# Kernel optimization log

Hardware: AMD Instinct MI355X
Metric: run time of the kernel (lower is better)

The kernel has to match this reference:

```python
import jax, jax.numpy as jnp
import numpy as np
from jax import lax

THRESHOLD = 0.95
NUM_HEADS = 32
Q_HEAD_DIM = 96
K_DIM = 1024
EPS = 1e-8


def dynamic_token_replacement(emb, thr=THRESHOLD):
    """Greedy sequential merge: token j is replaced by the first earlier
    *unused* token i with cosine sim > thr. emb: (S, D) -> (S, D)."""
    S = emb.shape[0]
    norm = jnp.maximum(jnp.linalg.norm(emb, axis=-1, keepdims=True), EPS)
    n = emb / norm
    sim = n @ n.T  # (S, S) cosine similarity
    idx = jnp.arange(S)

    def step(carry, xs):
        used, rep = carry
        i, row = xs
        # i can only absorb later, unused tokens, and only if i itself is unused
        cand = (idx > i) & (row > thr) & (~used) & (~used[i])
        rep = jnp.where(cand, i, rep)
        used = used | cand
        return (used, rep), None

    (used, rep), _ = lax.scan(step, (jnp.zeros(S, bool), idx), (idx, sim))
    return emb[rep]


def setup_inputs() -> dict:
    key = jax.random.key(0)
    ks = jax.random.split(key, 7)
    B, S, D = 2, 1024, 3072
    s = 0.02
    return {
        "hidden_states": jax.random.normal(ks[0], (B, S, D), jnp.float32),
        "Wq": jax.random.normal(ks[1], (D, D), jnp.float32) * s,
        "bq": jnp.zeros((D,), jnp.float32),
        "Wk": jax.random.normal(ks[2], (D, K_DIM), jnp.float32) * s,
        "bk": jnp.zeros((K_DIM,), jnp.float32),
        "Wv": jax.random.normal(ks[3], (D, K_DIM), jnp.float32) * s,
        "bv": jnp.zeros((K_DIM,), jnp.float32),
        "Wqk": jax.random.normal(ks[4], (Q_HEAD_DIM, K_DIM), jnp.float32) * s,
        "bqk": jnp.zeros((K_DIM,), jnp.float32),
        "Wo": jax.random.normal(ks[5], (K_DIM, D), jnp.float32) * s,
        "bo": jnp.zeros((D,), jnp.float32),
    }


def reference(hidden_states, Wq, bq, Wk, bk, Wv, bv, Wqk, bqk, Wo, bo):
    B, S, D = hidden_states.shape
    q = hidden_states @ Wq + bq                      # (B, S, 3072)
    k = hidden_states @ Wk + bk                      # (B, S, 1024)
    v = hidden_states @ Wv + bv                      # (B, S, 1024)

    q = q.reshape(B, S, NUM_HEADS, Q_HEAD_DIM).transpose(0, 2, 1, 3)  # (B, H, S, 96)
    q_new = q @ Wqk + bqk                            # (B, H, S, 1024)

    new_k = jax.vmap(dynamic_token_replacement)(k)   # (B, S, 1024)
    new_v = jax.vmap(dynamic_token_replacement)(v)   # (B, S, 1024)

    scale = 1.0 / jnp.sqrt(jnp.float32(K_DIM))
    scores = jnp.einsum('bhsk,btk->bhst', q_new, new_k) * scale  # (B, H, S, S)
    attn = jax.nn.softmax(scores, axis=-1)
    out = jnp.einsum('bhst,btk->bhsk', attn, new_v)  # (B, H, S, 1024)
    out = out.mean(axis=1)                           # (B, S, 1024)
    return out @ Wo + bo                             # (B, S, 3072)
```

## Files before the change

### kernel.cpp

```cpp
#include <hip/hip_runtime.h>
#include <hip/hip_bf16.h>
#include <stdint.h>

#define BATCH 2
#define SEQ   1024
#define DIM   3072
#define KDIM  1024
#define NHEAD 32
#define HDQ   96
#define THR_SIM 0.95f

typedef unsigned short u16;
typedef __attribute__((ext_vector_type(8))) short short8;
typedef __attribute__((ext_vector_type(4))) float f32x4;

typedef const __attribute__((address_space(1))) unsigned int* gas_ptr;
typedef __attribute__((address_space(3))) unsigned int* las_ptr;

__device__ __forceinline__ void glds16(const u16* g, u16* l) {
  __builtin_amdgcn_global_load_lds((gas_ptr)g, (las_ptr)l, 16, 0, 0);
}

__device__ __forceinline__ u16 f2bf(float f) {
  union { float f; unsigned u; } v; v.f = f;
  unsigned r = v.u + 0x7FFFu + ((v.u >> 16) & 1u);
  return (u16)(r >> 16);
}
__device__ __forceinline__ float bf2f(u16 x) {
  union { unsigned u; float f; } v; v.u = ((unsigned)x) << 16; return v.f;
}

__device__ __forceinline__ f32x4 mfma16(short8 a, short8 b, f32x4 c) {
  return __builtin_amdgcn_mfma_f32_16x16x32_bf16(a, b, c, 0, 0, 0);
}

__global__ void k_cvt_bf16(const float* __restrict__ in, u16* __restrict__ out, int n4) {
  int i = blockIdx.x * blockDim.x + threadIdx.x;
  if (i < n4) {
    float4 v = ((const float4*)in)[i];
    ushort4 o;
    o.x = f2bf(v.x); o.y = f2bf(v.y); o.z = f2bf(v.z); o.w = f2bf(v.w);
    ((ushort4*)out)[i] = o;
  }
}

__global__ void k_tr_f32_bf16(const float* __restrict__ in, u16* __restrict__ out, int R, int C) {
  __shared__ float t[32][33];
  int c0 = blockIdx.x * 32, r0 = blockIdx.y * 32;
  int tx = threadIdx.x, ty = threadIdx.y;
  #pragma unroll
  for (int k = 0; k < 4; ++k)
    t[ty + 8 * k][tx] = in[(size_t)(r0 + ty + 8 * k) * C + c0 + tx];
  __syncthreads();
  #pragma unroll
  for (int k = 0; k < 4; ++k)
    out[(size_t)(c0 + ty + 8 * k) * R + r0 + tx] = f2bf(t[tx][ty + 8 * k]);
}

__global__ void k_tr_bf16(const u16* __restrict__ in, u16* __restrict__ out,
                          int ldin, int ldout, long long zsIn, long long zsOut) {
  __shared__ u16 t[32][33];
  const u16* ib = in + (size_t)blockIdx.z * zsIn;
  u16* ob = out + (size_t)blockIdx.z * zsOut;
  int c0 = blockIdx.x * 32, r0 = blockIdx.y * 32;
  int tx = threadIdx.x, ty = threadIdx.y;
  #pragma unroll
  for (int k = 0; k < 4; ++k)
    t[ty + 8 * k][tx] = ib[(size_t)(r0 + ty + 8 * k) * ldin + c0 + tx];
  __syncthreads();
  #pragma unroll
  for (int k = 0; k < 4; ++k)
    ob[(size_t)(c0 + ty + 8 * k) * ldout + r0 + tx] = t[tx][ty + 8 * k];
}

__global__ void k_build_wqke(const float* __restrict__ Wqk, const float* __restrict__ bqk,
                             u16* __restrict__ out) {
  const int n = blockIdx.x;
  const int c = threadIdx.x * 4;
  float4 v;
  if (n < 96)       v = *(const float4*)(Wqk + (size_t)n * KDIM + c);
  else if (n == 96) v = *(const float4*)(bqk + c);
  else              v = make_float4(0.f, 0.f, 0.f, 0.f);
  ushort4 o;
  o.x = f2bf(v.x); o.y = f2bf(v.y); o.z = f2bf(v.z); o.w = f2bf(v.w);
  *(ushort4*)(out + (size_t)n * KDIM + c) = o;
}

__global__ void k_bkv(const float* __restrict__ bk, const float* __restrict__ bv,
                      float* __restrict__ out) {
  int i = blockIdx.x * 256 + threadIdx.x;
  if (i < 2048) out[i] = (i < 1024) ? bk[i] : bv[i - 1024];
}

template<bool OUT_BF16, bool BIAS>
__global__ __launch_bounds__(256, 3) void k_gemm_bt(
    const u16* __restrict__ A, const u16* __restrict__ Bt, void* __restrict__ Cv,
    const float* __restrict__ bias, int M, int N, int K,
    int lda, int ldb, int ldc,
    long long bsAH, long long bsAL, long long bsBH, long long bsBL,
    long long bsCH, long long bsCL)
{
  const int zb = blockIdx.y, zH = zb >> 1, zL = zb & 1;
  A  += (size_t)(zH * bsAH + zL * bsAL);
  Bt += (size_t)(zH * bsBH + zL * bsBL);
  u16*   Cb16 = (u16*)Cv + (size_t)(zH * bsCH + zL * bsCL);
  float* Cf32 = (float*)Cv + (size_t)(zH * bsCH + zL * bsCL);

  __shared__ u16 Ls[2][24 * 512];
  const int nt = N >> 6;
  int bid = blockIdx.x;
  {
    const int nwg = gridDim.x;
    const int qq = nwg >> 3, rr = nwg & 7;
    const int x = bid & 7, pos = bid >> 3;
    bid = (x < rr ? x * (qq + 1) : rr * (qq + 1) + (x - rr) * qq) + pos;
  }
  const int tm = bid / nt, tn = bid % nt;
  const int tid = threadIdx.x, lane = tid & 63, wid = tid >> 6;
  const int wr = wid >> 1, wc = wid & 1, li = lane & 15, lg = lane >> 4;

  const int rsub = lane >> 3;
  const int cbe = ((lane & 7) ^ rsub) << 3;
  const u16* gp[6];
  int lof[6];
  #pragma unroll
  for (int j = 0; j < 6; ++j) {
    const int ci = wid * 6 + j;
    lof[j] = ci << 9;
    if (ci < 16) gp[j] = A + (size_t)(tm * 128 + ci * 8 + rsub) * lda + cbe;
    else         gp[j] = Bt + (size_t)(tn * 64 + (ci - 16) * 8 + rsub) * ldb + cbe;
  }

  f32x4 acc[4][2];
  #pragma unroll
  for (int a = 0; a < 4; ++a)
    #pragma unroll
    for (int b = 0; b < 2; ++b) acc[a][b] = (f32x4){0.f, 0.f, 0.f, 0.f};

  const int nk = K >> 6;
  #pragma unroll
  for (int j = 0; j < 6; ++j) { glds16(gp[j], Ls[0] + lof[j]); gp[j] += 64; }
  __syncthreads();

  for (int kt = 0; kt < nk; ++kt) {
    const u16* Lc = Ls[kt & 1];
    if (kt + 1 < nk) {
      u16* Ln = Ls[(kt + 1) & 1];
      #pragma unroll
      for (int j = 0; j < 6; ++j) { glds16(gp[j], Ln + lof[j]); gp[j] += 64; }
    }
    short8 af[2][4], bfv[2][2];
    #pragma unroll
    for (int ks = 0; ks < 2; ++ks) {
      const int sw = (((ks * 4 + lg) ^ (li & 7)) << 3);
      #pragma unroll
      for (int mf = 0; mf < 4; ++mf)
        af[ks][mf] = *(const short8*)(Lc + (wr * 64 + mf * 16 + li) * 64 + sw);
      #pragma unroll
      for (int nf = 0; nf < 2; ++nf)
        bfv[ks][nf] = *(const short8*)(Lc + 8192 + (wc * 32 + nf * 16 + li) * 64 + sw);
    }
    #pragma unroll
    for (int ks = 0; ks < 2; ++ks)
      #pragma unroll
      for (int mf = 0; mf < 4; ++mf)
        #pragma unroll
        for (int nf = 0; nf < 2; ++nf)
          acc[mf][nf] = mfma16(af[ks][mf], bfv[ks][nf], acc[mf][nf]);
    __syncthreads();
  }
  #pragma unroll
  for (int mf = 0; mf < 4; ++mf) {
    #pragma unroll
    for (int nf = 0; nf < 2; ++nf) {
      const int col = tn * 64 + wc * 32 + nf * 16 + li;
      const float bb = BIAS ? bias[col] : 0.f;
      #pragma unroll
      for (int j = 0; j < 4; ++j) {
        const int row = tm * 128 + wr * 64 + mf * 16 + lg * 4 + j;
        const float v = acc[mf][nf][j] + bb;
        if (OUT_BF16) Cb16[(size_t)row * ldc + col] = f2bf(v);
        else          Cf32[(size_t)row * ldc + col] = v;
      }
    }
  }
}

__global__ void k_norms(const float* __restrict__ gram, float* __restrict__ nrm,
                        int* __restrict__ anyCnt) {
  const int s = blockIdx.x, j = threadIdx.x;
  const float* g = gram + (size_t)s * SEQ * SEQ;
  float nj = fmaxf(sqrtf(fmaxf(g[(size_t)j * SEQ + j], 0.f)), 1e-8f);
  nrm[s * SEQ + j] = nj;
  if (j == 0) anyCnt[s] = 0;
}

__global__ void k_rowany(const float* __restrict__ gram, const float* __restrict__ nrm,
                         unsigned char* __restrict__ rowAny, int* __restrict__ anyCnt) {
  const int i = blockIdx.x, s = blockIdx.y, t = threadIdx.x;
  const float* g = gram + (size_t)s * SEQ * SEQ + (size_t)i * SEQ;
  const float* nr = nrm + s * SEQ;
  const float ni = nr[i];
  int any = 0;
  for (int j = i + 1 + t; j < SEQ; j += 256)
    any |= (g[j] > THR_SIM * ni * nr[j]) ? 1 : 0;
  any = __any(any) ? 1 : 0;
  __shared__ int sh[4];
  if ((t & 63) == 0) sh[t >> 6] = any;
  __syncthreads();
  if (t == 0) {
    int a = sh[0] | sh[1] | sh[2] | sh[3];
    rowAny[s * SEQ + i] = (unsigned char)a;
    if (a) atomicAdd(&anyCnt[s], 1);
  }
}

__global__ __launch_bounds__(1024) void k_scan_replace(
    const float* __restrict__ gram, const float* __restrict__ nrmG,
    const unsigned char* __restrict__ rowAnyG, const int* __restrict__ anyCnt,
    u16* __restrict__ kvbase)
{
  const int s = blockIdx.x;
  if (anyCnt[s] == 0) return;
  const float* g = gram + (size_t)s * SEQ * SEQ;
  u16* dat = kvbase + (size_t)(s >> 1) * (2048 * 2048 / 2) * 2 + (size_t)(s & 1) * 1024;
  const int ldr = 2048;
  __shared__ float nrm[SEQ];
  __shared__ unsigned char used[SEQ];
  __shared__ unsigned char rowAny[SEQ];
  __shared__ short rep[SEQ];
  const int j = threadIdx.x;
  nrm[j] = nrmG[s * SEQ + j];
  rowAny[j] = rowAnyG[s * SEQ + j];
  used[j] = 0; rep[j] = (short)j;
  __syncthreads();
  for (int i = 0; i < SEQ - 1; ++i) {
    if (rowAny[i] && !used[i]) {
      const float t = THR_SIM * nrm[i];
      if (j > i && !used[j] && g[(size_t)i * SEQ + j] > t * nrm[j]) {
        used[j] = 1; rep[j] = (short)i;
      }
      __syncthreads();
    }
  }
  __syncthreads();
  const int src = rep[j];
  if (src != j) {
    for (int c = 0; c < KDIM; c += 8)
      *(uint4*)(dat + (size_t)j * ldr + c) = *(const uint4*)(dat + (size_t)src * ldr + c);
  }
}

__global__ __launch_bounds__(1024, 4) void k_attn3(
    const u16* __restrict__ q_bf, const u16* __restrict__ KKTe,
    u16* __restrict__ pbarP)
{
  const int bid = blockIdx.x;
  const int xcd = bid & 7, qt = bid >> 3;
  const int b = xcd >> 2, pg = xcd & 3;
  const int q0 = qt * 16;
  const int tid = threadIdx.x, lane = tid & 63, w = tid >> 6;
  const int li = lane & 15, lg = lane >> 4;

  __shared__ float bkkl[1024];
  __shared__ float2 red[2][16][16];

  const u16* KKb = KKTe + (size_t)b * SEQ * 128;
  bkkl[tid] = bf2f(KKb[(size_t)tid * 128 + 96]);

  short8 ak[4][3];
  #pragma unroll
  for (int kf = 0; kf < 4; ++kf)
    #pragma unroll
    for (int ks = 0; ks < 3; ++ks)
      ak[kf][ks] = *(const short8*)(KKb + (size_t)(w * 64 + kf * 16 + li) * 128 + ks * 32 + lg * 8);

  f32x4 accm[4];
  #pragma unroll
  for (int kf = 0; kf < 4; ++kf) accm[kf] = (f32x4){0.f, 0.f, 0.f, 0.f};
  __syncthreads();

  const u16* qrow = q_bf + (size_t)(b * SEQ + q0 + li) * DIM + pg * 8 * HDQ;

  for (int hh = 0; hh < 8; ++hh) {
    const u16* qp = qrow + hh * HDQ;
    f32x4 acc[4];
    #pragma unroll
    for (int kf = 0; kf < 4; ++kf) acc[kf] = (f32x4){0.f, 0.f, 0.f, 0.f};
    #pragma unroll
    for (int ks = 0; ks < 3; ++ks) {
      short8 bq = *(const short8*)(qp + ks * 32 + lg * 8);
      #pragma unroll
      for (int kf = 0; kf < 4; ++kf)
        acc[kf] = mfma16(ak[kf][ks], bq, acc[kf]);
    }
    float m = -1e30f;
    #pragma unroll
    for (int kf = 0; kf < 4; ++kf) {
      f32x4 bb = *(const f32x4*)(bkkl + w * 64 + kf * 16 + lg * 4);
      #pragma unroll
      for (int j = 0; j < 4; ++j) {
        float s = (acc[kf][j] + bb[j]) * 0.03125f;
        acc[kf][j] = s;
        m = fmaxf(m, s);
      }
    }
    m = fmaxf(m, __shfl_xor(m, 16));
    m = fmaxf(m, __shfl_xor(m, 32));
    float ssum = 0.f;
    #pragma unroll
    for (int kf = 0; kf < 4; ++kf)
      #pragma unroll
      for (int j = 0; j < 4; ++j) {
        float pv = __expf(acc[kf][j] - m);
        acc[kf][j] = pv;
        ssum += pv;
      }
    ssum += __shfl_xor(ssum, 16);
    ssum += __shfl_xor(ssum, 32);
    if (lane < 16) red[hh & 1][w][li] = make_float2(m, ssum);
    __syncthreads();
    float mg = -1e30f;
    #pragma unroll
    for (int ww = 0; ww < 16; ++ww) mg = fmaxf(mg, red[hh & 1][ww][li].x);
    float Sg = 0.f;
    #pragma unroll
    for (int ww = 0; ww < 16; ++ww) {
      float2 msv = red[hh & 1][ww][li];
      Sg += msv.y * __expf(msv.x - mg);
    }
    const float gi = __expf(m - mg) / (32.f * Sg);
    #pragma unroll
    for (int kf = 0; kf < 4; ++kf)
      #pragma unroll
      for (int j = 0; j < 4; ++j)
        accm[kf][j] += acc[kf][j] * gi;
  }

  u16* dst = pbarP + (size_t)(pg * 2 + b) * SEQ * SEQ + (size_t)(q0 + li) * SEQ + w * 64;
  #pragma unroll
  for (int kf = 0; kf < 4; ++kf) {
    ushort4 o;
    o.x = f2bf(accm[kf][0]); o.y = f2bf(accm[kf][1]);
    o.z = f2bf(accm[kf][2]); o.w = f2bf(accm[kf][3]);
    *(ushort4*)(dst + kf * 16 + lg * 4) = o;
  }
}

__global__ void k_reduce_pbar(const u16* __restrict__ part, u16* __restrict__ out) {
  const size_t N = (size_t)BATCH * SEQ * SEQ;
  size_t i = (size_t)blockIdx.x * blockDim.x + threadIdx.x;
  if (i >= N / 8) return;
  short8 p0 = ((const short8*)part)[i];
  short8 p1 = ((const short8*)(part + N))[i];
  short8 p2 = ((const short8*)(part + 2 * N))[i];
  short8 p3 = ((const short8*)(part + 3 * N))[i];
  short8 o;
  #pragma unroll
  for (int j = 0; j < 8; ++j) {
    float s = bf2f((u16)p0[j]) + bf2f((u16)p1[j]) + bf2f((u16)p2[j]) + bf2f((u16)p3[j]);
    o[j] = (short)f2bf(s);
  }
  ((short8*)out)[i] = o;
}

extern "C" void kernel_launch(void* const* d_in, const int* in_sizes, int n_in,
                              void* d_out, int out_size, void* d_ws, size_t ws_size,
                              hipStream_t stream)
{
  (void)in_sizes; (void)n_in; (void)out_size;
  const float* hs  = (const float*)d_in[0];
  const float* Wq  = (const float*)d_in[1];
  const float* bq  = (const float*)d_in[2];
  const float* Wk  = (const float*)d_in[3];
  const float* bk  = (const float*)d_in[4];
  const float* Wv  = (const float*)d_in[5];
  const float* bv  = (const float*)d_in[6];
  const float* Wqk = (const float*)d_in[7];
  const float* bqk = (const float*)d_in[8];
  const float* Wo  = (const float*)d_in[9];
  const float* bo  = (const float*)d_in[10];

  char* p = (char*)d_ws;
  u16*   hs_bf   = (u16*)(p + 0);
  float* gram4   = (float*)(p + 0);
  u16*   pbarP   = (u16*)(p + 0);
  u16*   WqT     = (u16*)(p + 12582912);
  u16*   WkvT    = (u16*)(p + 12582912);
  u16*   WqkE    = (u16*)(p + 16777216);
  u16*   KKTe    = (u16*)(p + 17039360);
  u16*   vTb     = (u16*)(p + 17563648);
  u16*   WoT     = (u16*)(p + 21757952);
  u16*   q_bf    = (u16*)(p + 31457280);
  u16*   kv_bf   = (u16*)(p + 44040192);
  u16*   Pbar_bf = (u16*)(p + 44040192);
  u16*   pv_out  = (u16*)(p + 48234496);
  float* bkv     = (float*)(p + 52428800);
  float* nrm4    = (float*)(p + 52436992);
  unsigned char* rowAny4 = (unsigned char*)(p + 52453376);
  int*   anyCnt  = (int*)(p + 52457472);
  if (ws_size < 58916864) return;

  const dim3 tb(32, 8);
  const long long SS = (long long)SEQ * SEQ;
  const long long KVB = 2048LL * 1024;

  k_cvt_bf16<<<6144, 256, 0, stream>>>(hs, hs_bf, BATCH * SEQ * DIM / 4);
  k_tr_f32_bf16<<<dim3(96, 96), tb, 0, stream>>>(Wq, WqT, DIM, DIM);
  k_gemm_bt<true, true><<<dim3(768, 1), 256, 0, stream>>>(hs_bf, WqT, q_bf, bq,
      2048, DIM, DIM, DIM, DIM, DIM, 0, 0, 0, 0, 0, 0);
  k_tr_f32_bf16<<<dim3(32, 96), tb, 0, stream>>>(Wk, WkvT, DIM, KDIM);
  k_tr_f32_bf16<<<dim3(32, 96), tb, 0, stream>>>(Wv, WkvT + (size_t)1024 * DIM, DIM, KDIM);
  k_bkv<<<8, 256, 0, stream>>>(bk, bv, bkv);
  k_gemm_bt<true, true><<<dim3(512, 1), 256, 0, stream>>>(hs_bf, WkvT, kv_bf, bkv,
      2048, 2048, DIM, DIM, DIM, 2048, 0, 0, 0, 0, 0, 0);
  k_gemm_bt<false, false><<<dim3(128, 4), 256, 0, stream>>>(kv_bf, kv_bf, gram4, nullptr,
      SEQ, SEQ, KDIM, 2048, 2048, SEQ,
      KVB, 1024, KVB, 1024, 2 * SS, SS);
  k_norms<<<4, 1024, 0, stream>>>(gram4, nrm4, anyCnt);
  k_rowany<<<dim3(SEQ, 4), 256, 0, stream>>>(gram4, nrm4, rowAny4, anyCnt);
  k_scan_replace<<<4, 1024, 0, stream>>>(gram4, nrm4, rowAny4, anyCnt, kv_bf);
  k_build_wqke<<<128, 256, 0, stream>>>(Wqk, bqk, WqkE);
  k_gemm_bt<true, false><<<dim3(16, 2), 256, 0, stream>>>(kv_bf, WqkE, KKTe, nullptr,
      SEQ, 128, KDIM, 2048, KDIM, 128, 0, KVB, 0, 0, 0, (long long)SEQ * 128);
  k_tr_bf16<<<dim3(32, 32, 2), tb, 0, stream>>>(kv_bf + 1024, vTb, 2048, SEQ, KVB, SS);
  k_tr_f32_bf16<<<dim3(96, 32), tb, 0, stream>>>(Wo, WoT, KDIM, DIM);
  k_attn3<<<512, 1024, 0, stream>>>(q_bf, KKTe, pbarP);
  k_reduce_pbar<<<1024, 256, 0, stream>>>(pbarP, Pbar_bf);
  k_gemm_bt<true, false><<<dim3(128, 2), 256, 0, stream>>>(Pbar_bf, vTb, pv_out, nullptr,
      SEQ, KDIM, SEQ, SEQ, SEQ, KDIM, 0, SS, 0, SS, 0, SS);
  k_gemm_bt<false, true><<<dim3(768, 1), 256, 0, stream>>>(pv_out, WoT, (float*)d_out, bo,
      2048, DIM, KDIM, KDIM, KDIM, DIM, 0, 0, 0, 0, 0, 0);
}
```

Baseline: 251.0 us.

## Two-pass softmax without max subtraction, fold scale and log2e into Wqk

The 1/32 score scale and log2(e) are folded into the bf16 Wqk/bqk extension, so the kernel can use exp2 directly. The attention kernel now runs two passes over the heads. The first computes only the per-head softmax denominators, skipping the running max and letting a single block barrier replace the per-head syncs. The second recomputes the MFMA scores and accumulates normalized probabilities, trading redundant MFMA and exp work for fewer barriers and less reduction traffic, at the risk of overflow without max subtraction. The launch-bounds occupancy hint also drops from 4 to 2.

```diff
diff --git a/kernel.cpp b/kernel.cpp
--- a/kernel.cpp
+++ b/kernel.cpp
@@ -77,12 +77,13 @@
                              u16* __restrict__ out) {
   const int n = blockIdx.x;
   const int c = threadIdx.x * 4;
+  const float sc = 0.03125f * 1.44269504f;
   float4 v;
   if (n < 96)       v = *(const float4*)(Wqk + (size_t)n * KDIM + c);
   else if (n == 96) v = *(const float4*)(bqk + c);
   else              v = make_float4(0.f, 0.f, 0.f, 0.f);
   ushort4 o;
-  o.x = f2bf(v.x); o.y = f2bf(v.y); o.z = f2bf(v.z); o.w = f2bf(v.w);
+  o.x = f2bf(v.x * sc); o.y = f2bf(v.y * sc); o.z = f2bf(v.z * sc); o.w = f2bf(v.w * sc);
   *(ushort4*)(out + (size_t)n * KDIM + c) = o;
 }
 
@@ -251,7 +252,7 @@
   }
 }
 
-__global__ __launch_bounds__(1024, 4) void k_attn3(
+__global__ __launch_bounds__(1024, 2) void k_attn4(
     const u16* __restrict__ q_bf, const u16* __restrict__ KKTe,
     u16* __restrict__ pbarP)
 {
@@ -263,7 +264,7 @@
   const int li = lane & 15, lg = lane >> 4;
 
   __shared__ float bkkl[1024];
-  __shared__ float2 red[2][16][16];
+  __shared__ float red[16][16][8];
 
   const u16* KKb = KKTe + (size_t)b * SEQ * 128;
   bkkl[tid] = bf2f(KKb[(size_t)tid * 128 + 96]);
@@ -274,10 +275,6 @@
     #pragma unroll
     for (int ks = 0; ks < 3; ++ks)
       ak[kf][ks] = *(const short8*)(KKb + (size_t)(w * 64 + kf * 16 + li) * 128 + ks * 32 + lg * 8);
-
-  f32x4 accm[4];
-  #pragma unroll
-  for (int kf = 0; kf < 4; ++kf) accm[kf] = (f32x4){0.f, 0.f, 0.f, 0.f};
   __syncthreads();
 
   const u16* qrow = q_bf + (size_t)(b * SEQ + q0 + li) * DIM + pg * 8 * HDQ;
@@ -294,47 +291,58 @@
       for (int kf = 0; kf < 4; ++kf)
         acc[kf] = mfma16(ak[kf][ks], bq, acc[kf]);
     }
-    float m = -1e30f;
+    float ssum = 0.f;
     #pragma unroll
     for (int kf = 0; kf < 4; ++kf) {
-      f32x4 bb = *(const f32x4*)(bkkl + w * 64 + kf * 16 + lg * 4);
-      #pragma unroll
-      for (int j = 0; j < 4; ++j) {
-        float s = (acc[kf][j] + bb[j]) * 0.03125f;
-        acc[kf][j] = s;
-        m = fmaxf(m, s);
-      }
-    }
-    m = fmaxf(m, __shfl_xor(m, 16));
-    m = fmaxf(m, __shfl_xor(m, 32));
-    float ssum = 0.f;
-    #pragma unroll
-    for (int kf = 0; kf < 4; ++kf)
-      #pragma unroll
-      for (int j = 0; j < 4; ++j) {
-        float pv = __expf(acc[kf][j] - m);
-        acc[kf][j] = pv;
-        ssum += pv;
-      }
+      f32x4 bb = *(const f32x4*)(&bkkl[w * 64 + kf * 16 + lg * 4]);
+      #pragma unroll
+      for (int j = 0; j < 4; ++j)
+        ssum += exp2f(acc[kf][j] + bb[j]);
+    }
     ssum += __shfl_xor(ssum, 16);
     ssum += __shfl_xor(ssum, 32);
-    if (lane < 16) red[hh & 1][w][li] = make_float2(m, ssum);
-    __syncthreads();
-    float mg = -1e30f;
-    #pragma unroll
-    for (int ww = 0; ww < 16; ++ww) mg = fmaxf(mg, red[hh & 1][ww][li].x);
-    float Sg = 0.f;
+    if (lane < 16) red[w][li][hh] = ssum;
+  }
+  __syncthreads();
+
+  float gi[8];
+  {
+    f32x4 s0 = (f32x4){0.f, 0.f, 0.f, 0.f}, s1 = (f32x4){0.f, 0.f, 0.f, 0.f};
     #pragma unroll
     for (int ww = 0; ww < 16; ++ww) {
-      float2 msv = red[hh & 1][ww][li];
-      Sg += msv.y * __expf(msv.x - mg);
-    }
-    const float gi = __expf(m - mg) / (32.f * Sg);
-    #pragma unroll
-    for (int kf = 0; kf < 4; ++kf)
+      s0 += *(const f32x4*)(&red[ww][li][0]);
+      s1 += *(const f32x4*)(&red[ww][li][4]);
+    }
+    #pragma unroll
+    for (int j = 0; j < 4; ++j) {
+      gi[j]     = __builtin_amdgcn_rcpf(32.f * s0[j]);
+      gi[4 + j] = __builtin_amdgcn_rcpf(32.f * s1[j]);
+    }
+  }
+
+  f32x4 accm[4];
+  #pragma unroll
+  for (int kf = 0; kf < 4; ++kf) accm[kf] = (f32x4){0.f, 0.f, 0.f, 0.f};
+  for (int hh = 0; hh < 8; ++hh) {
+    const u16* qp = qrow + hh * HDQ;
+    f32x4 acc[4];
+    #pragma unroll
+    for (int kf = 0; kf < 4; ++kf) acc[kf] = (f32x4){0.f, 0.f, 0.f, 0.f};
+    #pragma unroll
+    for (int ks = 0; ks < 3; ++ks) {
+      short8 bq = *(const short8*)(qp + ks * 32 + lg * 8);
+      #pragma unroll
+      for (int kf = 0; kf < 4; ++kf)
+        acc[kf] = mfma16(ak[kf][ks], bq, acc[kf]);
+    }
+    const float g = gi[hh];
+    #pragma unroll
+    for (int kf = 0; kf < 4; ++kf) {
+      f32x4 bb = *(const f32x4*)(&bkkl[w * 64 + kf * 16 + lg * 4]);
       #pragma unroll
       for (int j = 0; j < 4; ++j)
-        accm[kf][j] += acc[kf][j] * gi;
+        accm[kf][j] += exp2f(acc[kf][j] + bb[j]) * g;
+    }
   }
 
   u16* dst = pbarP + (size_t)(pg * 2 + b) * SEQ * SEQ + (size_t)(q0 + li) * SEQ + w * 64;
@@ -425,7 +433,7 @@
       SEQ, 128, KDIM, 2048, KDIM, 128, 0, KVB, 0, 0, 0, (long long)SEQ * 128);
   k_tr_bf16<<<dim3(32, 32, 2), tb, 0, stream>>>(kv_bf + 1024, vTb, 2048, SEQ, KVB, SS);
   k_tr_f32_bf16<<<dim3(96, 32), tb, 0, stream>>>(Wo, WoT, KDIM, DIM);
-  k_attn3<<<512, 1024, 0, stream>>>(q_bf, KKTe, pbarP);
+  k_attn4<<<512, 1024, 0, stream>>>(q_bf, KKTe, pbarP);
   k_reduce_pbar<<<1024, 256, 0, stream>>>(pbarP, Pbar_bf);
   k_gemm_bt<true, false><<<dim3(128, 2), 256, 0, stream>>>(Pbar_bf, vTb, pv_out, nullptr,
       SEQ, KDIM, SEQ, SEQ, SEQ, KDIM, 0, SS, 0, SS, 0, SS);
```

New measurement: 346.1 us. 1.38x slower.
